# Optimization experiments

Hardware: AMD Instinct MI355X
Metric: run time of the kernel (lower is better)

## Reference

```python
import jax, jax.numpy as jnp
import numpy as np

N = 16384            # number of input vectors
CODEBOOK_SIZE = 8192  # M
DIM = 256             # dim_feature
BETA = 0.25           # commitment_weight


def setup_inputs() -> dict:
    key = jax.random.key(0)
    kx, ke = jax.random.split(key)
    x = jax.random.normal(kx, (N, DIM), dtype=jnp.float32)
    # kaiming-uniform-style init for the codebook
    bound = float(np.sqrt(3.0 / DIM))
    embeddings = jax.random.uniform(ke, (CODEBOOK_SIZE, DIM), dtype=jnp.float32,
                                    minval=-bound, maxval=bound)
    return {"x": x, "embeddings": embeddings}


def reference(x, embeddings):
    # l2_dist: sqrt(sum((x_i - e_j)^2)) computed via the GEMM expansion
    x2 = jnp.sum(x * x, axis=1, keepdims=True)               # (N, 1)
    e2 = jnp.sum(embeddings * embeddings, axis=1)            # (M,)
    d2 = x2 + e2[None, :] - 2.0 * (x @ embeddings.T)         # (N, M)
    dist = jnp.sqrt(jnp.maximum(d2, 0.0))
    # deterministic gumbel_sample path (training eval / stochastic=False):
    # argmax of logits = -dist  <=>  argmin of dist
    ind = jnp.argmin(dist, axis=1)                           # (N,)
    quantized = embeddings[ind]                              # one_hot @ embeddings
    # commitment loss: beta * ||x_q - sg(x)||^2 (docstring)
    commit_loss = BETA * jnp.mean((quantized - jax.lax.stop_gradient(x)) ** 2)
    # straight-through estimator
    quantized_st = x + jax.lax.stop_gradient(quantized - x)
    # perplexity from per-code counts (one-hot scatter)
    counts = jnp.zeros((CODEBOOK_SIZE,), jnp.float32).at[ind].add(1.0)
    probs = counts / counts.sum()
    perplexity = jnp.exp(-jnp.sum(probs * jnp.log(probs + 1e-10)))
    return quantized_st, ind, commit_loss, perplexity
```

## Files before the change

### kernel.cpp

```cpp
#include <hip/hip_runtime.h>
#include <stdint.h>


#define N_VEC 16384
#define M_CODES 8192
#define DIM 256
#define BETA 0.25f

#define NSLICE 4
#define SLICE_CODES 2048
#define BM 128
#define BN 128
#define NPART 8

#define BUFBYTES 32768
#define LDS_TOTAL (2 * BUFBYTES)
#define NSTEPS 128

typedef __attribute__((ext_vector_type(4))) float f32x4;
typedef __attribute__((ext_vector_type(8))) __bf16 bf16x8;

__device__ __forceinline__ void gll16(const void* g, const void* lds_p) {
    __builtin_amdgcn_global_load_lds(
        (const __attribute__((address_space(1))) uint32_t*)(uintptr_t)g,
        (__attribute__((address_space(3))) uint32_t*)(uint32_t)(uintptr_t)lds_p,
        16, 0, 0);
}
#define SB0() __builtin_amdgcn_sched_barrier(0)

__device__ __forceinline__ ushort f2bf(float f) {
    uint32_t u = __float_as_uint(f);
    return (ushort)((u + 0x7FFFu + ((u >> 16) & 1u)) >> 16);
}
__device__ __forceinline__ float bf2f(ushort h) {
    return __uint_as_float(((uint32_t)h) << 16);
}

__global__ __launch_bounds__(256) void prep_kernel(
    const float* __restrict__ x, const float* __restrict__ emb,
    ushort* __restrict__ xh, ushort* __restrict__ xl,
    ushort* __restrict__ eh, ushort* __restrict__ el,
    float* __restrict__ e2, unsigned* __restrict__ counts,
    float* __restrict__ loss_acc) {
    if (blockIdx.x < 8) {
        int4 z = {0, 0, 0, 0};
        ((int4*)counts)[blockIdx.x * 256 + threadIdx.x] = z;
        if (blockIdx.x == 0 && threadIdx.x == 0) *loss_acc = 0.0f;
    }
    const int wave = threadIdx.x >> 6;
    const int lane = threadIdx.x & 63;
    const int row = blockIdx.x * 4 + wave;

    const float* src;
    ushort* ph;
    ushort* pl;
    bool is_e;
    int er = row - N_VEC;
    if (row < N_VEC) {
        src = x + (size_t)row * DIM;
        ph = xh + (size_t)row * DIM;
        pl = xl + (size_t)row * DIM;
        is_e = false;
    } else {
        src = emb + (size_t)er * DIM;
        ph = eh + (size_t)er * DIM;
        pl = el + (size_t)er * DIM;
        is_e = true;
    }
    float4 v = *(const float4*)(src + lane * 4);
    ushort h0 = f2bf(v.x), h1 = f2bf(v.y), h2 = f2bf(v.z), h3 = f2bf(v.w);
    ushort l0 = f2bf(v.x - bf2f(h0)), l1 = f2bf(v.y - bf2f(h1));
    ushort l2 = f2bf(v.z - bf2f(h2)), l3 = f2bf(v.w - bf2f(h3));
    *(ushort4*)(ph + lane * 4) = make_ushort4(h0, h1, h2, h3);
    *(ushort4*)(pl + lane * 4) = make_ushort4(l0, l1, l2, l3);
    if (is_e) {
        float s = v.x * v.x + v.y * v.y + v.z * v.z + v.w * v.w;
        #pragma unroll
        for (int off = 32; off; off >>= 1) s += __shfl_xor(s, off);
        if (lane == 0) e2[er] = s;
    }
}

__global__ __launch_bounds__(256, 2) void vq_mfma_kernel(
    const ushort* __restrict__ xh, const ushort* __restrict__ xl,
    const ushort* __restrict__ eh, const ushort* __restrict__ el,
    const float* __restrict__ e2g, unsigned long long* __restrict__ partials) {
    extern __shared__ char lds[];

    const int t = threadIdx.x;
    const int lane = t & 63;
    const int wv = t >> 6;
    const int lane15 = lane & 15;
    const int l16 = lane >> 4;

    const int rt = blockIdx.x & 127;
    const int slice = blockIdx.x >> 7;
    const int row0 = rt * BM;
    const int cslice0 = slice * SLICE_CODES;

    const int wr0 = (wv & 1) * 64;
    const int wch = wv >> 1;

    const int swz = ((l16 ^ (lane15 >> 1)) & 3) << 4;
    const int byteA0 = (wr0 + lane15) * 64 + swz;
    const int byteB0 = (wch * 64 + lane15) * 64 + swz;

    const int s0 = wv * 128 + lane;
    const int s1 = s0 + 64;
    const int r0s = s0 >> 2, r1s = s1 >> 2;
    const int c0s = ((s0 & 3) ^ ((s0 >> 3) & 3)) << 3;
    const int c1s = ((s1 & 3) ^ ((s1 >> 3) & 3)) << 3;

    const ushort* pxh_a = xh + (size_t)(row0 + r0s) * DIM + c0s;
    const ushort* pxh_b = xh + (size_t)(row0 + r1s) * DIM + c1s;
    const ushort* pxl_a = xl + (size_t)(row0 + r0s) * DIM + c0s;
    const ushort* pxl_b = xl + (size_t)(row0 + r1s) * DIM + c1s;
    const ushort* peh_a = eh + (size_t)(cslice0 + r0s) * DIM + c0s;
    const ushort* peh_b = eh + (size_t)(cslice0 + r1s) * DIM + c1s;
    const ushort* pel_a = el + (size_t)(cslice0 + r0s) * DIM + c0s;
    const ushort* pel_b = el + (size_t)(cslice0 + r1s) * DIM + c1s;
    const int wdst = wv * 2048;

    auto stage = [&](int bufOff, int s) {
        char* b = lds + bufOff + wdst;
        const int xo = (s & 7) * 32;
        const size_t eo = ((size_t)(s >> 3) << 15) + (s & 7) * 32;
        gll16(pxh_a + xo, b);
        gll16(pxh_b + xo, b + 1024);
        gll16(pxl_a + xo, b + 8192);
        gll16(pxl_b + xo, b + 8192 + 1024);
        gll16(peh_a + eo, b + 16384);
        gll16(peh_b + eo, b + 16384 + 1024);
        gll16(pel_a + eo, b + 24576);
        gll16(pel_b + eo, b + 24576 + 1024);
    };

    float best[16];
    int bidx[16];
    #pragma unroll
    for (int s = 0; s < 16; ++s) { best[s] = __uint_as_float(0x7f800000u); bidx[s] = 0; }

    f32x4 acc[4][4];
    #pragma unroll
    for (int fi = 0; fi < 4; ++fi)
        #pragma unroll
        for (int fj = 0; fj < 4; ++fj) acc[fi][fj] = (f32x4){0.f, 0.f, 0.f, 0.f};

    float e2r[4];

    stage(0, 0); SB0();

    for (int s = 0; s < NSTEPS; ++s) {
        asm volatile("s_waitcnt vmcnt(0)" ::: "memory");
        __builtin_amdgcn_s_barrier();
        SB0();
        if (s + 1 < NSTEPS) { stage(((s + 1) & 1) * BUFBYTES, s + 1); SB0(); }
        if ((s & 7) == 0) {
            const int cb = cslice0 + (s >> 3) * BN + wch * 64 + lane15;
            #pragma unroll
            for (int fj = 0; fj < 4; ++fj) e2r[fj] = e2g[cb + fj * 16];
            SB0();
        }

        const char* lb = lds + (s & 1) * BUFBYTES;
        bf16x8 ah[4], alo[4];
        #pragma unroll
        for (int f = 0; f < 4; ++f) {
            ah[f] = *(const bf16x8*)(lb + byteA0 + f * 1024);
            alo[f] = *(const bf16x8*)(lb + 8192 + byteA0 + f * 1024);
        }
        __builtin_amdgcn_s_setprio(1);
        #pragma unroll
        for (int fj = 0; fj < 4; ++fj) {
            bf16x8 bh = *(const bf16x8*)(lb + 16384 + byteB0 + fj * 1024);
            bf16x8 blo = *(const bf16x8*)(lb + 24576 + byteB0 + fj * 1024);
            #pragma unroll
            for (int fi = 0; fi < 4; ++fi)
                acc[fi][fj] = __builtin_amdgcn_mfma_f32_16x16x32_bf16(
                    ah[fi], bh, acc[fi][fj], 0, 0, 0);
            #pragma unroll
            for (int fi = 0; fi < 4; ++fi)
                acc[fi][fj] = __builtin_amdgcn_mfma_f32_16x16x32_bf16(
                    ah[fi], blo, acc[fi][fj], 0, 0, 0);
            #pragma unroll
            for (int fi = 0; fi < 4; ++fi)
                acc[fi][fj] = __builtin_amdgcn_mfma_f32_16x16x32_bf16(
                    alo[fi], bh, acc[fi][fj], 0, 0, 0);
        }
        __builtin_amdgcn_s_setprio(0);

        if ((s & 7) == 7) {
            const int ct = s >> 3;
            const int cb = cslice0 + ct * BN + wch * 64 + lane15;
            #pragma unroll
            for (int fj = 0; fj < 4; ++fj) {
                const int c = cb + fj * 16;
                #pragma unroll
                for (int fi = 0; fi < 4; ++fi)
                    #pragma unroll
                    for (int r = 0; r < 4; ++r) {
                        float sc = e2r[fj] - 2.0f * acc[fi][fj][r];
                        const int slot = fi * 4 + r;
                        if (sc < best[slot]) { best[slot] = sc; bidx[slot] = c; }
                    }
            }
            #pragma unroll
            for (int fi = 0; fi < 4; ++fi)
                #pragma unroll
                for (int fj = 0; fj < 4; ++fj)
                    acc[fi][fj] = (f32x4){0.f, 0.f, 0.f, 0.f};
        }
    }

    #pragma unroll
    for (int slot = 0; slot < 16; ++slot) {
        float v = best[slot];
        int ix = bidx[slot];
        #pragma unroll
        for (int off = 1; off < 16; off <<= 1) {
            float v2 = __shfl_xor(v, off);
            int ix2 = __shfl_xor(ix, off);
            if (v2 < v || (v2 == v && ix2 < ix)) { v = v2; ix = ix2; }
        }
        if (lane15 == 0) {
            int fi = slot >> 2, r = slot & 3;
            int row = row0 + wr0 + fi * 16 + l16 * 4 + r;
            uint32_t u = __float_as_uint(v);
            uint32_t ord = (u & 0x80000000u) ? ~u : (u | 0x80000000u);
            partials[(size_t)(slice * 2 + wch) * N_VEC + row] =
                ((unsigned long long)ord << 32) | (unsigned)ix;
        }
    }
}

__global__ __launch_bounds__(256) void finish_kernel(
    const float* __restrict__ x, const float* __restrict__ emb,
    const unsigned long long* __restrict__ partials,
    float* __restrict__ out_ind, float* __restrict__ out_q,
    unsigned* __restrict__ counts, float* __restrict__ loss_acc) {
    __shared__ float partial[4];
    const int wave = threadIdx.x >> 6;
    const int lane = threadIdx.x & 63;
    const int row = blockIdx.x * 4 + wave;

    unsigned long long m = ~0ull;
    if (lane < NPART) m = partials[(size_t)lane * N_VEC + row];
    #pragma unroll
    for (int off = 1; off < NPART; off <<= 1) {
        unsigned long long v = __shfl_xor(m, off);
        if (v < m) m = v;
    }
    m = __shfl(m, 0);
    const int ix = (int)(unsigned)(m & 0xFFFFFFFFull);

    float4 q = *(const float4*)(emb + (size_t)ix * DIM + lane * 4);
    float4 xv = *(const float4*)(x + (size_t)row * DIM + lane * 4);
    *(float4*)(out_q + (size_t)row * DIM + lane * 4) = q;
    float dx = q.x - xv.x, dy = q.y - xv.y, dz = q.z - xv.z, dw = q.w - xv.w;
    float s = dx * dx + dy * dy + dz * dz + dw * dw;
    #pragma unroll
    for (int off = 32; off; off >>= 1) s += __shfl_xor(s, off);
    if (lane == 0) {
        out_ind[row] = (float)ix;
        atomicAdd(&counts[ix], 1u);
        partial[wave] = s;
    }
    __syncthreads();
    if (threadIdx.x == 0)
        atomicAdd(loss_acc, partial[0] + partial[1] + partial[2] + partial[3]);
}

__global__ __launch_bounds__(256) void finalize_kernel(
    const unsigned* __restrict__ counts, const float* __restrict__ loss_acc,
    float* __restrict__ out_scalars) {
    __shared__ float red[256];
    float h = 0.0f;
    for (int c = threadIdx.x; c < M_CODES; c += 256) {
        float p = (float)counts[c] * (1.0f / (float)N_VEC);
        h += p * logf(p + 1e-10f);
    }
    red[threadIdx.x] = h;
    __syncthreads();
    for (int s = 128; s; s >>= 1) {
        if (threadIdx.x < s) red[threadIdx.x] += red[threadIdx.x + s];
        __syncthreads();
    }
    if (threadIdx.x == 0) {
        out_scalars[0] = BETA * loss_acc[0] / (float)(N_VEC * DIM);
        out_scalars[1] = expf(-red[0]);
    }
}

extern "C" void kernel_launch(void* const* d_in, const int* in_sizes, int n_in,
                              void* d_out, int out_size, void* d_ws, size_t ws_size,
                              hipStream_t stream) {
    const float* x = (const float*)d_in[0];
    const float* emb = (const float*)d_in[1];

    float* out = (float*)d_out;
    float* out_q = out;
    float* out_ind = out + (size_t)N_VEC * DIM;
    float* out_scalars = out_ind + N_VEC;

    ushort* xh = (ushort*)out;
    ushort* xl = xh + (size_t)N_VEC * DIM;

    char* wp = (char*)d_ws;
    ushort* eh = (ushort*)wp;  wp += (size_t)M_CODES * DIM * 2;
    ushort* el = (ushort*)wp;  wp += (size_t)M_CODES * DIM * 2;
    float* e2 = (float*)wp;    wp += (size_t)M_CODES * 4;
    unsigned long long* partials = (unsigned long long*)wp;
    wp += (size_t)NPART * N_VEC * 8;
    unsigned* counts = (unsigned*)wp; wp += (size_t)M_CODES * 4;
    float* loss_acc = (float*)wp;

    prep_kernel<<<(N_VEC + M_CODES) / 4, 256, 0, stream>>>(x, emb, xh, xl, eh, el,
                                                           e2, counts, loss_acc);

    hipFuncSetAttribute((const void*)vq_mfma_kernel,
                        hipFuncAttributeMaxDynamicSharedMemorySize, LDS_TOTAL);
    vq_mfma_kernel<<<(N_VEC / BM) * NSLICE, 256, LDS_TOTAL, stream>>>(
        xh, xl, eh, el, e2, partials);

    finish_kernel<<<N_VEC / 4, 256, 0, stream>>>(x, emb, partials, out_ind, out_q,
                                                 counts, loss_acc);
    finalize_kernel<<<1, 256, 0, stream>>>(counts, loss_acc, out_scalars);
}
```

Measured before the change: 265.1 us.

## Use 8 waves per block with 32x64 per-wave tiles in VQ GEMM

Doubles the block to 512 threads (8 waves), so each wave covers a 32-row by 64-code sub-tile instead of 64x64. The staging plan changes from two to one 16-byte global-to-LDS load per thread per buffer. Per-wave accumulator and best/index register state is halved to allow more resident waves and better latency hiding. In exchange, each wave reads the B fragments from LDS for half as many MFMAs, which raises LDS traffic per FLOP, and the launch bound now asks for 4 blocks of 512 threads per CU while LDS use stays at 64KB per block.

Measured after the change: 262.9 us. Within noise of the previous version (-0.8%).

```diff
diff --git a/kernel.cpp b/kernel.cpp
--- a/kernel.cpp
+++ b/kernel.cpp
@@ -81,7 +81,7 @@
     }
 }
 
-__global__ __launch_bounds__(256, 2) void vq_mfma_kernel(
+__global__ __launch_bounds__(512, 4) void vq_mfma_kernel(
     const ushort* __restrict__ xh, const ushort* __restrict__ xl,
     const ushort* __restrict__ eh, const ushort* __restrict__ el,
     const float* __restrict__ e2g, unsigned long long* __restrict__ partials) {
@@ -98,51 +98,40 @@
     const int row0 = rt * BM;
     const int cslice0 = slice * SLICE_CODES;
 
-    const int wr0 = (wv & 1) * 64;
-    const int wch = wv >> 1;
+    const int wr0 = (wv & 3) * 32;
+    const int wch = wv >> 2;
 
     const int swz = ((l16 ^ (lane15 >> 1)) & 3) << 4;
     const int byteA0 = (wr0 + lane15) * 64 + swz;
     const int byteB0 = (wch * 64 + lane15) * 64 + swz;
 
-    const int s0 = wv * 128 + lane;
-    const int s1 = s0 + 64;
-    const int r0s = s0 >> 2, r1s = s1 >> 2;
-    const int c0s = ((s0 & 3) ^ ((s0 >> 3) & 3)) << 3;
-    const int c1s = ((s1 & 3) ^ ((s1 >> 3) & 3)) << 3;
-
-    const ushort* pxh_a = xh + (size_t)(row0 + r0s) * DIM + c0s;
-    const ushort* pxh_b = xh + (size_t)(row0 + r1s) * DIM + c1s;
-    const ushort* pxl_a = xl + (size_t)(row0 + r0s) * DIM + c0s;
-    const ushort* pxl_b = xl + (size_t)(row0 + r1s) * DIM + c1s;
-    const ushort* peh_a = eh + (size_t)(cslice0 + r0s) * DIM + c0s;
-    const ushort* peh_b = eh + (size_t)(cslice0 + r1s) * DIM + c1s;
-    const ushort* pel_a = el + (size_t)(cslice0 + r0s) * DIM + c0s;
-    const ushort* pel_b = el + (size_t)(cslice0 + r1s) * DIM + c1s;
-    const int wdst = wv * 2048;
+    const int rs = t >> 2;
+    const int cs = ((t & 3) ^ ((t >> 3) & 3)) << 3;
+
+    const ushort* pxh = xh + (size_t)(row0 + rs) * DIM + cs;
+    const ushort* pxl = xl + (size_t)(row0 + rs) * DIM + cs;
+    const ushort* peh = eh + (size_t)(cslice0 + rs) * DIM + cs;
+    const ushort* pel = el + (size_t)(cslice0 + rs) * DIM + cs;
+    const int wdst = wv * 1024;
 
     auto stage = [&](int bufOff, int s) {
         char* b = lds + bufOff + wdst;
         const int xo = (s & 7) * 32;
         const size_t eo = ((size_t)(s >> 3) << 15) + (s & 7) * 32;
-        gll16(pxh_a + xo, b);
-        gll16(pxh_b + xo, b + 1024);
-        gll16(pxl_a + xo, b + 8192);
-        gll16(pxl_b + xo, b + 8192 + 1024);
-        gll16(peh_a + eo, b + 16384);
-        gll16(peh_b + eo, b + 16384 + 1024);
-        gll16(pel_a + eo, b + 24576);
-        gll16(pel_b + eo, b + 24576 + 1024);
+        gll16(pxh + xo, b);
+        gll16(pxl + xo, b + 8192);
+        gll16(peh + eo, b + 16384);
+        gll16(pel + eo, b + 24576);
     };
 
-    float best[16];
-    int bidx[16];
-    #pragma unroll
-    for (int s = 0; s < 16; ++s) { best[s] = __uint_as_float(0x7f800000u); bidx[s] = 0; }
-
-    f32x4 acc[4][4];
-    #pragma unroll
-    for (int fi = 0; fi < 4; ++fi)
+    float best[8];
+    int bidx[8];
+    #pragma unroll
+    for (int s = 0; s < 8; ++s) { best[s] = __uint_as_float(0x7f800000u); bidx[s] = 0; }
+
+    f32x4 acc[2][4];
+    #pragma unroll
+    for (int fi = 0; fi < 2; ++fi)
         #pragma unroll
         for (int fj = 0; fj < 4; ++fj) acc[fi][fj] = (f32x4){0.f, 0.f, 0.f, 0.f};
 
@@ -163,9 +152,9 @@
         }
 
         const char* lb = lds + (s & 1) * BUFBYTES;
-        bf16x8 ah[4], alo[4];
-        #pragma unroll
-        for (int f = 0; f < 4; ++f) {
+        bf16x8 ah[2], alo[2];
+        #pragma unroll
+        for (int f = 0; f < 2; ++f) {
             ah[f] = *(const bf16x8*)(lb + byteA0 + f * 1024);
             alo[f] = *(const bf16x8*)(lb + 8192 + byteA0 + f * 1024);
         }
@@ -175,15 +164,15 @@
             bf16x8 bh = *(const bf16x8*)(lb + 16384 + byteB0 + fj * 1024);
             bf16x8 blo = *(const bf16x8*)(lb + 24576 + byteB0 + fj * 1024);
             #pragma unroll
-            for (int fi = 0; fi < 4; ++fi)
+            for (int fi = 0; fi < 2; ++fi)
                 acc[fi][fj] = __builtin_amdgcn_mfma_f32_16x16x32_bf16(
                     ah[fi], bh, acc[fi][fj], 0, 0, 0);
             #pragma unroll
-            for (int fi = 0; fi < 4; ++fi)
+            for (int fi = 0; fi < 2; ++fi)
                 acc[fi][fj] = __builtin_amdgcn_mfma_f32_16x16x32_bf16(
                     ah[fi], blo, acc[fi][fj], 0, 0, 0);
             #pragma unroll
-            for (int fi = 0; fi < 4; ++fi)
+            for (int fi = 0; fi < 2; ++fi)
                 acc[fi][fj] = __builtin_amdgcn_mfma_f32_16x16x32_bf16(
                     alo[fi], bh, acc[fi][fj], 0, 0, 0);
         }
@@ -196,7 +185,7 @@
             for (int fj = 0; fj < 4; ++fj) {
                 const int c = cb + fj * 16;
                 #pragma unroll
-                for (int fi = 0; fi < 4; ++fi)
+                for (int fi = 0; fi < 2; ++fi)
                     #pragma unroll
                     for (int r = 0; r < 4; ++r) {
                         float sc = e2r[fj] - 2.0f * acc[fi][fj][r];
@@ -205,7 +194,7 @@
                     }
             }
             #pragma unroll
-            for (int fi = 0; fi < 4; ++fi)
+            for (int fi = 0; fi < 2; ++fi)
                 #pragma unroll
                 for (int fj = 0; fj < 4; ++fj)
                     acc[fi][fj] = (f32x4){0.f, 0.f, 0.f, 0.f};
@@ -213,7 +202,7 @@
     }
 
     #pragma unroll
-    for (int slot = 0; slot < 16; ++slot) {
+    for (int slot = 0; slot < 8; ++slot) {
         float v = best[slot];
         int ix = bidx[slot];
         #pragma unroll
@@ -319,7 +308,7 @@
 
     hipFuncSetAttribute((const void*)vq_mfma_kernel,
                         hipFuncAttributeMaxDynamicSharedMemorySize, LDS_TOTAL);
-    vq_mfma_kernel<<<(N_VEC / BM) * NSLICE, 256, LDS_TOTAL, stream>>>(
+    vq_mfma_kernel<<<(N_VEC / BM) * NSLICE, 512, LDS_TOTAL, stream>>>(
         xh, xl, eh, el, e2, partials);
 
     finish_kernel<<<N_VEC / 4, 256, 0, stream>>>(x, emb, partials, out_ind, out_q,
```
